# Optimization experiments

Measured on AMD Instinct MI355X. Metric: run time of the kernel, lower is better.

Reference implementation:

```python
import jax, jax.numpy as jnp
import numpy as np

B, L, D, H = 4, 2048, 512, 8
DK = D // H


def setup_inputs() -> dict:
    key = jax.random.key(0)
    ks = jax.random.split(key, 12)
    s = 1.0 / np.sqrt(D)
    return {
        "q": jax.random.normal(ks[0], (B, L, D), jnp.float32),
        "k": jax.random.normal(ks[1], (B, L, D), jnp.float32),
        "v": jax.random.normal(ks[2], (B, L, D), jnp.float32),
        "masks": jax.random.randint(ks[3], (B, L), 0, 2, jnp.int32),
        "wq_w": jax.random.normal(ks[4], (D, D), jnp.float32) * s,
        "wq_b": jnp.zeros((D,), jnp.float32),
        "wk_w": jax.random.normal(ks[5], (D, D), jnp.float32) * s,
        "wk_b": jnp.zeros((D,), jnp.float32),
        "wv_w": jax.random.normal(ks[6], (D, D), jnp.float32) * s,
        "wv_b": jnp.zeros((D,), jnp.float32),
        "wo_w": jax.random.normal(ks[7], (D, D), jnp.float32) * s,
        "wo_b": jnp.zeros((D,), jnp.float32),
    }


def reference(q, k, v, masks, wq_w, wq_b, wk_w, wk_b, wv_w, wv_b, wo_w, wo_b):
    b, l1, d = q.shape
    l2 = k.shape[1]
    # torch Linear: y = x @ W.T + b; weight shape (out, in)
    qh = (q @ wq_w.T + wq_b).reshape(b, l1, H, DK).transpose(0, 2, 1, 3)  # (B,H,L1,DK)
    kh = (k @ wk_w.T + wk_b).reshape(b, l2, H, DK).transpose(0, 2, 1, 3)  # (B,H,L2,DK)
    vh = (v @ wv_w.T + wv_b).reshape(b, l2, H, DK).transpose(0, 2, 1, 3)  # (B,H,L2,DK)
    scores = jnp.einsum("bhqd,bhkd->bhqk", qh, kh) / np.sqrt(DK).astype(np.float32)
    # 2D encoder mask (B, L2) broadcast over heads and query positions
    neg = jnp.float32(np.finfo(np.float32).min)
    scores = jnp.where(masks[:, None, None, :] == 0, neg, scores)
    weights = jax.nn.softmax(scores, axis=-1)  # dropout_rate=0.0 -> identity
    ctx = jnp.einsum("bhqk,bhkd->bhqd", weights, vh)
    concat = ctx.transpose(0, 2, 1, 3).reshape(b, l1, d)
    return concat @ wo_w.T + wo_b
```

## Files before the change

kernel.cpp:

```cpp
#include <hip/hip_runtime.h>
#include <hip/hip_bf16.h>
#include <cstddef>

typedef __attribute__((ext_vector_type(8)))  short bf16x8;
typedef __attribute__((ext_vector_type(4)))  short bf16x4;
typedef __attribute__((ext_vector_type(4)))  float f32x4;

constexpr int Bn = 4, Ln = 2048, Dn = 512, Hn = 8, DKn = 64, Mtot = 8192;
constexpr float QSCALE = 0.125f * 1.44269504088896341f;
constexpr size_t HE = (size_t)Bn * Hn * Ln * DKn;
constexpr size_t WN = (size_t)Dn * Dn;

__device__ inline unsigned cvt_pk_bf16(float lo, float hi) {
    unsigned r;
    asm("v_cvt_pk_bf16_f32 %0, %1, %2" : "=v"(r) : "v"(lo), "v"(hi));
    return r;
}
__device__ inline short f2bf(float x) {
    union { float f; unsigned u; } v; v.f = x;
    unsigned r = v.u + 0x7fffu + ((v.u >> 16) & 1u);
    return (short)(r >> 16);
}
__device__ inline void gl_lds16(const short* g, short* l) {
    __builtin_amdgcn_global_load_lds(
        (const __attribute__((address_space(1))) void*)g,
        (__attribute__((address_space(3))) void*)l, 16, 0, 0);
}

__global__ __launch_bounds__(256) void prep_all(
    const float* __restrict__ q, const float* __restrict__ k, const float* __restrict__ v,
    const float* __restrict__ wq, const float* __restrict__ wk,
    const float* __restrict__ wv, const float* __restrict__ wo,
    const int* __restrict__ masks,
    short* __restrict__ Xb, short* __restrict__ Wb, float* __restrict__ maskF)
{
    const size_t NX4 = 3 * HE / 4;
    const size_t NW4 = WN;
    size_t gid = (size_t)blockIdx.x * 256 + threadIdx.x;
    if (gid < NX4) {
        const size_t per = HE / 4;
        int which = (int)(gid >> 20);
        const float* src = (which == 0) ? q : (which == 1) ? k : v;
        size_t i4 = gid & (per - 1);
        float4 xv = *(const float4*)&src[i4 * 4];
        uint2 p = {cvt_pk_bf16(xv.x, xv.y), cvt_pk_bf16(xv.z, xv.w)};
        *(uint2*)&Xb[(size_t)which * HE + i4 * 4] = p;
    } else if (gid < NX4 + NW4) {
        size_t wi4 = gid - NX4;
        const size_t per = WN / 4;
        int which = (int)(wi4 >> 16);
        const float* src = (which == 0) ? wq : (which == 1) ? wk : (which == 2) ? wv : wo;
        size_t i4 = wi4 & (per - 1);
        float4 xv = *(const float4*)&src[i4 * 4];
        uint2 p = {cvt_pk_bf16(xv.x, xv.y), cvt_pk_bf16(xv.z, xv.w)};
        *(uint2*)&Wb[(size_t)which * WN + i4 * 4] = p;
    } else {
        size_t mi = gid - NX4 - NW4;
        if (mi < (size_t)Bn * Ln) maskF[mi] = (masks[mi] == 0) ? -1e30f : 0.f;
    }
}

__global__ __launch_bounds__(256) void mask_prep(
    const int* __restrict__ masks, float* __restrict__ maskF)
{
    int i = blockIdx.x * 256 + threadIdx.x;
    if (i < Bn * Ln) maskF[i] = (masks[i] == 0) ? -1e30f : 0.f;
}

__global__ __launch_bounds__(256) void qkv_proj_bf16(
    const short* __restrict__ Xb, const short* __restrict__ Wb,
    const float* __restrict__ bq, const float* __restrict__ bk, const float* __restrict__ bv,
    short* __restrict__ Qh, short* __restrict__ Kh, short* __restrict__ Vt)
{
    const int p = blockIdx.z;
    const short* X    = Xb + (size_t)p * Mtot * Dn;
    const short* W    = Wb + (size_t)p * Dn * Dn;
    const float* bias = (p == 0) ? bq : (p == 1) ? bk : bv;
    short*       O    = (p == 0) ? Qh : (p == 1) ? Kh : Vt;
    const float scl   = (p == 0) ? QSCALE : 1.0f;

    __shared__ short As[128 * 64];
    __shared__ short Bs[128 * 64];

    const int tid  = threadIdx.x;
    const int lane = tid & 63, w = tid >> 6;
    const int wr = w >> 1, wc = w & 1;
    const int l16 = lane & 15, g = lane >> 4;
    const int m0 = blockIdx.x * 128, n0 = blockIdx.y * 128;

    const short* Ag[4]; const short* Bg[4]; int ldsOff[4];
    #pragma unroll
    for (int f = 0; f < 4; ++f) {
        int c = tid + 256 * f;
        int row = c >> 3, col8 = c & 7;
        int scolw = ((col8 ^ (row & 7)) << 3);
        Ag[f] = X + (size_t)(m0 + row) * Dn + scolw;
        Bg[f] = W + (size_t)(n0 + row) * Dn + scolw;
        ldsOff[f] = (w * 64 + 256 * f) * 8;
    }

    f32x4 acc[4][4];
    #pragma unroll
    for (int i = 0; i < 4; ++i)
        #pragma unroll
        for (int j = 0; j < 4; ++j)
            acc[i][j] = (f32x4){0.f, 0.f, 0.f, 0.f};

    for (int ks = 0; ks < 8; ++ks) {
        #pragma unroll
        for (int f = 0; f < 4; ++f) {
            gl_lds16(Ag[f], &As[ldsOff[f]]);
            gl_lds16(Bg[f], &Bs[ldsOff[f]]);
            Ag[f] += 64; Bg[f] += 64;
        }
        __syncthreads();

        bf16x8 bfv[4][2];
        #pragma unroll
        for (int j = 0; j < 4; ++j) {
            int row = wc * 64 + j * 16 + l16;
            int sw = (row & 7) << 3;
            bfv[j][0] = *(const bf16x8*)&Bs[row * 64 + ((g * 8) ^ sw)];
            bfv[j][1] = *(const bf16x8*)&Bs[row * 64 + ((32 + g * 8) ^ sw)];
        }
        #pragma unroll
        for (int i = 0; i < 4; ++i) {
            int row = wr * 64 + i * 16 + l16;
            int sw = (row & 7) << 3;
            bf16x8 a0 = *(const bf16x8*)&As[row * 64 + ((g * 8) ^ sw)];
            bf16x8 a1 = *(const bf16x8*)&As[row * 64 + ((32 + g * 8) ^ sw)];
            #pragma unroll
            for (int j = 0; j < 4; ++j) {
                acc[i][j] = __builtin_amdgcn_mfma_f32_16x16x32_bf16(a0, bfv[j][0], acc[i][j], 0, 0, 0);
                acc[i][j] = __builtin_amdgcn_mfma_f32_16x16x32_bf16(a1, bfv[j][1], acc[i][j], 0, 0, 0);
            }
        }
        __syncthreads();
    }

    const int bb = m0 >> 11;
    #pragma unroll
    for (int i = 0; i < 4; ++i) {
        #pragma unroll
        for (int j = 0; j < 4; ++j) {
            int n  = n0 + wc * 64 + j * 16 + l16;
            int h  = n >> 6, dk = n & 63;
            float bval = bias[n];
            #pragma unroll
            for (int r = 0; r < 4; ++r) {
                int m  = m0 + wr * 64 + i * 16 + g * 4 + r;
                int lq = m & (Ln - 1);
                short val = f2bf((acc[i][j][r] + bval) * scl);
                if (p < 2)
                    O[(((size_t)bb * Hn + h) * Ln + lq) * DKn + dk] = val;
                else
                    O[(((size_t)bb * Hn + h) * DKn + dk) * Ln + lq] = val;
            }
        }
    }
}

__global__ __launch_bounds__(256) void out_proj_bf16(
    const short* __restrict__ Ctx, const short* __restrict__ Wo,
    const float* __restrict__ bias, float* __restrict__ Out)
{
    __shared__ short As[128 * 64];
    __shared__ short Bs[128 * 64];

    const int tid  = threadIdx.x;
    const int lane = tid & 63, w = tid >> 6;
    const int wr = w >> 1, wc = w & 1;
    const int l16 = lane & 15, g = lane >> 4;
    const int m0 = blockIdx.x * 128, n0 = blockIdx.y * 128;

    const short* Ag[4]; const short* Bg[4]; int ldsOff[4];
    #pragma unroll
    for (int f = 0; f < 4; ++f) {
        int c = tid + 256 * f;
        int row = c >> 3, col8 = c & 7;
        int scolw = ((col8 ^ (row & 7)) << 3);
        Ag[f] = Ctx + (size_t)(m0 + row) * Dn + scolw;
        Bg[f] = Wo  + (size_t)(n0 + row) * Dn + scolw;
        ldsOff[f] = (w * 64 + 256 * f) * 8;
    }

    f32x4 acc[4][4];
    #pragma unroll
    for (int i = 0; i < 4; ++i)
        #pragma unroll
        for (int j = 0; j < 4; ++j)
            acc[i][j] = (f32x4){0.f, 0.f, 0.f, 0.f};

    for (int ks = 0; ks < 8; ++ks) {
        #pragma unroll
        for (int f = 0; f < 4; ++f) {
            gl_lds16(Ag[f], &As[ldsOff[f]]);
            gl_lds16(Bg[f], &Bs[ldsOff[f]]);
            Ag[f] += 64; Bg[f] += 64;
        }
        __syncthreads();

        bf16x8 bfv[4][2];
        #pragma unroll
        for (int j = 0; j < 4; ++j) {
            int row = wc * 64 + j * 16 + l16;
            int sw = (row & 7) << 3;
            bfv[j][0] = *(const bf16x8*)&Bs[row * 64 + ((g * 8) ^ sw)];
            bfv[j][1] = *(const bf16x8*)&Bs[row * 64 + ((32 + g * 8) ^ sw)];
        }
        #pragma unroll
        for (int i = 0; i < 4; ++i) {
            int row = wr * 64 + i * 16 + l16;
            int sw = (row & 7) << 3;
            bf16x8 a0 = *(const bf16x8*)&As[row * 64 + ((g * 8) ^ sw)];
            bf16x8 a1 = *(const bf16x8*)&As[row * 64 + ((32 + g * 8) ^ sw)];
            #pragma unroll
            for (int j = 0; j < 4; ++j) {
                acc[i][j] = __builtin_amdgcn_mfma_f32_16x16x32_bf16(a0, bfv[j][0], acc[i][j], 0, 0, 0);
                acc[i][j] = __builtin_amdgcn_mfma_f32_16x16x32_bf16(a1, bfv[j][1], acc[i][j], 0, 0, 0);
            }
        }
        __syncthreads();
    }

    #pragma unroll
    for (int i = 0; i < 4; ++i) {
        #pragma unroll
        for (int j = 0; j < 4; ++j) {
            int n = n0 + wc * 64 + j * 16 + l16;
            float bval = bias[n];
            #pragma unroll
            for (int r = 0; r < 4; ++r) {
                int m = m0 + wr * 64 + i * 16 + g * 4 + r;
                Out[(size_t)m * Dn + n] = acc[i][j][r] + bval;
            }
        }
    }
}

__global__ __launch_bounds__(256, 4) void attn_mfma(
    const short* __restrict__ Qh, const short* __restrict__ Kh, const short* __restrict__ Vt,
    const float* __restrict__ maskF, short* __restrict__ Ctx)
{
    __shared__ short Ks[2][64 * 64];
    __shared__ short Vs[2][64 * 64];

    const int tid  = threadIdx.x;
    const int lane = tid & 63, w = tid >> 6;
    const int l16 = lane & 15, g = lane >> 4;

    const int bid = blockIdx.x;
    const int id  = (bid & 7) * 128 + (bid >> 3);
    const int qb  = id & 31;
    const int bh  = id >> 5;
    const int bb  = bh >> 3, h = bh & 7;
    const int q0  = qb * 64;
    const int NT  = Ln / 64;

    const short* Qp = Qh + (size_t)bh * Ln * DKn;
    const short* Kp = Kh + (size_t)bh * Ln * DKn;
    const short* Vp = Vt + (size_t)bh * DKn * Ln;
    const float* mp = maskF + bb * Ln;

    bf16x8 qf0 = *(const bf16x8*)&Qp[(size_t)(q0 + w * 16 + l16) * DKn + g * 8];
    bf16x8 qf1 = *(const bf16x8*)&Qp[(size_t)(q0 + w * 16 + l16) * DKn + 32 + g * 8];

    constexpr short BF1 = (short)0x3F80;
    const bf16x8 ones = {BF1, BF1, BF1, BF1, BF1, BF1, BF1, BF1};

    const int lrow = lane >> 3;
    const int scol = (((lane & 7) ^ lrow) << 3);
    const int p0r = (2 * w) * 8 + lrow, p1r = (2 * w + 1) * 8 + lrow;
    const int k0r = (p0r & 0x20) | ((p0r & 0x0C) << 1) | ((p0r & 0x10) >> 2) | (p0r & 3);
    const int k1r = (p1r & 0x20) | ((p1r & 0x0C) << 1) | ((p1r & 0x10) >> 2) | (p1r & 3);
    const short* kg0 = Kp + (size_t)k0r * DKn + scol;
    const short* kg1 = Kp + (size_t)k1r * DKn + scol;
    const short* vg0 = Vp + (size_t)p0r * Ln + scol;
    const short* vg1 = Vp + (size_t)p1r * Ln + scol;
    const int ldsb0 = (2 * w) * 512, ldsb1 = (2 * w + 1) * 512;

    int kofs[4][2];
    #pragma unroll
    for (int kt = 0; kt < 4; ++kt) {
        int row = kt * 16 + l16;
        kofs[kt][0] = row * 64 + ((g * 8) ^ ((row & 7) << 3));
        kofs[kt][1] = row * 64 + ((32 + g * 8) ^ ((row & 7) << 3));
    }

    f32x4 oacc[4];
    #pragma unroll
    for (int d = 0; d < 4; ++d) oacc[d] = (f32x4){0.f, 0.f, 0.f, 0.f};
    f32x4 lsum = (f32x4){0.f, 0.f, 0.f, 0.f};

    gl_lds16(kg0, &Ks[0][ldsb0]);
    gl_lds16(kg1, &Ks[0][ldsb1]);
    gl_lds16(vg0, &Vs[0][ldsb0]);
    gl_lds16(vg1, &Vs[0][ldsb1]);
    __syncthreads();

    int c = 0;
    for (int t = 0; t < NT; ++t) {
        if (t < NT - 1) {
            const int ko = (t + 1) * (64 * DKn);
            const int vo = (t + 1) * 64;
            gl_lds16(kg0 + ko, &Ks[c ^ 1][ldsb0]);
            gl_lds16(kg1 + ko, &Ks[c ^ 1][ldsb1]);
            gl_lds16(vg0 + vo, &Vs[c ^ 1][ldsb0]);
            gl_lds16(vg1 + vo, &Vs[c ^ 1][ldsb1]);
        }

        f32x4 mk[4];
        mk[0] = *(const f32x4*)&mp[t * 64 + 8 * g];
        mk[1] = *(const f32x4*)&mp[t * 64 + 8 * g + 4];
        mk[2] = *(const f32x4*)&mp[t * 64 + 32 + 8 * g];
        mk[3] = *(const f32x4*)&mp[t * 64 + 32 + 8 * g + 4];

        f32x4 sv[4];
        __builtin_amdgcn_s_setprio(1);
        #pragma unroll
        for (int kt = 0; kt < 4; ++kt) {
            bf16x8 kf0 = *(const bf16x8*)&Ks[c][kofs[kt][0]];
            bf16x8 kf1 = *(const bf16x8*)&Ks[c][kofs[kt][1]];
            f32x4 z = __builtin_amdgcn_mfma_f32_16x16x32_bf16(kf0, qf0, mk[kt], 0, 0, 0);
            z = __builtin_amdgcn_mfma_f32_16x16x32_bf16(kf1, qf1, z, 0, 0, 0);
            sv[kt] = z;
        }
        __builtin_amdgcn_s_setprio(0);

        bf16x8 pf[2];
        #pragma unroll
        for (int cc = 0; cc < 2; ++cc) {
            float e0 = exp2f(sv[2 * cc][0]), e1 = exp2f(sv[2 * cc][1]);
            float e2 = exp2f(sv[2 * cc][2]), e3 = exp2f(sv[2 * cc][3]);
            float e4 = exp2f(sv[2 * cc + 1][0]), e5 = exp2f(sv[2 * cc + 1][1]);
            float e6 = exp2f(sv[2 * cc + 1][2]), e7 = exp2f(sv[2 * cc + 1][3]);
            union { unsigned u[4]; bf16x8 v; } pu;
            pu.u[0] = cvt_pk_bf16(e0, e1);
            pu.u[1] = cvt_pk_bf16(e2, e3);
            pu.u[2] = cvt_pk_bf16(e4, e5);
            pu.u[3] = cvt_pk_bf16(e6, e7);
            pf[cc] = pu.v;
        }

        __builtin_amdgcn_s_setprio(1);
        #pragma unroll
        for (int cc = 0; cc < 2; ++cc) {
            lsum = __builtin_amdgcn_mfma_f32_16x16x32_bf16(ones, pf[cc], lsum, 0, 0, 0);
            #pragma unroll
            for (int d = 0; d < 4; ++d) {
                bf16x8 vf = *(const bf16x8*)&Vs[c][kofs[d][cc]];
                oacc[d] = __builtin_amdgcn_mfma_f32_16x16x32_bf16(vf, pf[cc], oacc[d], 0, 0, 0);
            }
        }
        __builtin_amdgcn_s_setprio(0);

        __syncthreads();
        c ^= 1;
    }

    float inv = 1.0f / lsum[0];
    size_t mrow = (size_t)bb * Ln + q0 + w * 16 + l16;
    #pragma unroll
    for (int d = 0; d < 4; ++d) {
        uint2 pr = {cvt_pk_bf16(oacc[d][0] * inv, oacc[d][1] * inv),
                    cvt_pk_bf16(oacc[d][2] * inv, oacc[d][3] * inv)};
        *(uint2*)&Ctx[mrow * Dn + h * 64 + d * 16 + g * 4] = pr;
    }
}

__global__ __launch_bounds__(256) void qkv_proj_mfma(
    const float* __restrict__ q, const float* __restrict__ k, const float* __restrict__ v,
    const float* __restrict__ wq, const float* __restrict__ wk, const float* __restrict__ wv,
    const float* __restrict__ bq, const float* __restrict__ bk, const float* __restrict__ bv,
    short* __restrict__ Qh, short* __restrict__ Kh, short* __restrict__ Vt)
{
    const int p = blockIdx.z;
    const float* X    = (p == 0) ? q  : (p == 1) ? k  : v;
    const float* W    = (p == 0) ? wq : (p == 1) ? wk : wv;
    const float* bias = (p == 0) ? bq : (p == 1) ? bk : bv;
    short*       O    = (p == 0) ? Qh : (p == 1) ? Kh : Vt;
    const float scl   = (p == 0) ? QSCALE : 1.0f;

    __shared__ short As[128 * 72];
    __shared__ short Bs[128 * 72];

    const int tid  = threadIdx.x;
    const int lane = tid & 63, w = tid >> 6;
    const int wr = w >> 1, wc = w & 1;
    const int l16 = lane & 15, g = lane >> 4;
    const int m0 = blockIdx.x * 128, n0 = blockIdx.y * 128;

    f32x4 acc[4][4];
    #pragma unroll
    for (int i = 0; i < 4; ++i)
        #pragma unroll
        for (int j = 0; j < 4; ++j)
            acc[i][j] = (f32x4){0.f, 0.f, 0.f, 0.f};

    for (int k0 = 0; k0 < Dn; k0 += 64) {
        #pragma unroll
        for (int f = 0; f < 8; ++f) {
            int lin = tid + 256 * f;
            int row = lin >> 4, c4 = lin & 15;
            float4 xv = *(const float4*)&X[(size_t)(m0 + row) * Dn + k0 + c4 * 4];
            uint2 xp = {cvt_pk_bf16(xv.x, xv.y), cvt_pk_bf16(xv.z, xv.w)};
            *(uint2*)&As[row * 72 + c4 * 4] = xp;
            float4 wv4 = *(const float4*)&W[(size_t)(n0 + row) * Dn + k0 + c4 * 4];
            uint2 wp = {cvt_pk_bf16(wv4.x, wv4.y), cvt_pk_bf16(wv4.z, wv4.w)};
            *(uint2*)&Bs[row * 72 + c4 * 4] = wp;
        }
        __syncthreads();

        bf16x8 af[4][2], bfv[4][2];
        #pragma unroll
        for (int i = 0; i < 4; ++i)
            #pragma unroll
            for (int c = 0; c < 2; ++c)
                af[i][c] = *(const bf16x8*)&As[(wr * 64 + i * 16 + l16) * 72 + c * 32 + g * 8];
        #pragma unroll
        for (int j = 0; j < 4; ++j)
            #pragma unroll
            for (int c = 0; c < 2; ++c)
                bfv[j][c] = *(const bf16x8*)&Bs[(wc * 64 + j * 16 + l16) * 72 + c * 32 + g * 8];

        #pragma unroll
        for (int i = 0; i < 4; ++i)
            #pragma unroll
            for (int j = 0; j < 4; ++j) {
                acc[i][j] = __builtin_amdgcn_mfma_f32_16x16x32_bf16(af[i][0], bfv[j][0], acc[i][j], 0, 0, 0);
                acc[i][j] = __builtin_amdgcn_mfma_f32_16x16x32_bf16(af[i][1], bfv[j][1], acc[i][j], 0, 0, 0);
            }
        __syncthreads();
    }

    const int bb = m0 >> 11;
    #pragma unroll
    for (int i = 0; i < 4; ++i) {
        #pragma unroll
        for (int j = 0; j < 4; ++j) {
            int n  = n0 + wc * 64 + j * 16 + l16;
            int h  = n >> 6, dk = n & 63;
            float bval = bias[n];
            #pragma unroll
            for (int r = 0; r < 4; ++r) {
                int m  = m0 + wr * 64 + i * 16 + g * 4 + r;
                int lq = m & (Ln - 1);
                short val = f2bf((acc[i][j][r] + bval) * scl);
                if (p < 2)
                    O[(((size_t)bb * Hn + h) * Ln + lq) * DKn + dk] = val;
                else
                    O[(((size_t)bb * Hn + h) * DKn + dk) * Ln + lq] = val;
            }
        }
    }
}

__global__ __launch_bounds__(256) void out_proj_mfma(
    const short* __restrict__ Ctx, const float* __restrict__ W,
    const float* __restrict__ bias, float* __restrict__ Out)
{
    __shared__ short As[128 * 72];
    __shared__ short Bs[128 * 72];

    const int tid  = threadIdx.x;
    const int lane = tid & 63, w = tid >> 6;
    const int wr = w >> 1, wc = w & 1;
    const int l16 = lane & 15, g = lane >> 4;
    const int m0 = blockIdx.x * 128, n0 = blockIdx.y * 128;

    f32x4 acc[4][4];
    #pragma unroll
    for (int i = 0; i < 4; ++i)
        #pragma unroll
        for (int j = 0; j < 4; ++j)
            acc[i][j] = (f32x4){0.f, 0.f, 0.f, 0.f};

    for (int k0 = 0; k0 < Dn; k0 += 64) {
        #pragma unroll
        for (int f = 0; f < 4; ++f) {
            int lin = tid + 256 * f;
            int row = lin >> 3, c8 = lin & 7;
            bf16x8 av = *(const bf16x8*)&Ctx[(size_t)(m0 + row) * Dn + k0 + c8 * 8];
            *(bf16x8*)&As[row * 72 + c8 * 8] = av;
        }
        #pragma unroll
        for (int f = 0; f < 8; ++f) {
            int lin = tid + 256 * f;
            int row = lin >> 4, c4 = lin & 15;
            float4 wv4 = *(const float4*)&W[(size_t)(n0 + row) * Dn + k0 + c4 * 4];
            uint2 wp = {cvt_pk_bf16(wv4.x, wv4.y), cvt_pk_bf16(wv4.z, wv4.w)};
            *(uint2*)&Bs[row * 72 + c4 * 4] = wp;
        }
        __syncthreads();

        bf16x8 af[4][2], bfv[4][2];
        #pragma unroll
        for (int i = 0; i < 4; ++i)
            #pragma unroll
            for (int c = 0; c < 2; ++c)
                af[i][c] = *(const bf16x8*)&As[(wr * 64 + i * 16 + l16) * 72 + c * 32 + g * 8];
        #pragma unroll
        for (int j = 0; j < 4; ++j)
            #pragma unroll
            for (int c = 0; c < 2; ++c)
                bfv[j][c] = *(const bf16x8*)&Bs[(wc * 64 + j * 16 + l16) * 72 + c * 32 + g * 8];

        #pragma unroll
        for (int i = 0; i < 4; ++i)
            #pragma unroll
            for (int j = 0; j < 4; ++j) {
                acc[i][j] = __builtin_amdgcn_mfma_f32_16x16x32_bf16(af[i][0], bfv[j][0], acc[i][j], 0, 0, 0);
                acc[i][j] = __builtin_amdgcn_mfma_f32_16x16x32_bf16(af[i][1], bfv[j][1], acc[i][j], 0, 0, 0);
            }
        __syncthreads();
    }

    #pragma unroll
    for (int i = 0; i < 4; ++i) {
        #pragma unroll
        for (int j = 0; j < 4; ++j) {
            int n = n0 + wc * 64 + j * 16 + l16;
            float bval = bias[n];
            #pragma unroll
            for (int r = 0; r < 4; ++r) {
                int m = m0 + wr * 64 + i * 16 + g * 4 + r;
                Out[(size_t)m * Dn + n] = acc[i][j][r] + bval;
            }
        }
    }
}

extern "C" void kernel_launch(void* const* d_in, const int* in_sizes, int n_in,
                              void* d_out, int out_size, void* d_ws, size_t ws_size,
                              hipStream_t stream)
{
    (void)in_sizes; (void)n_in; (void)out_size;
    const float* q    = (const float*)d_in[0];
    const float* k    = (const float*)d_in[1];
    const float* v    = (const float*)d_in[2];
    const int*   mks  = (const int*)  d_in[3];
    const float* wq_w = (const float*)d_in[4];
    const float* wq_b = (const float*)d_in[5];
    const float* wk_w = (const float*)d_in[6];
    const float* wk_b = (const float*)d_in[7];
    const float* wv_w = (const float*)d_in[8];
    const float* wv_b = (const float*)d_in[9];
    const float* wo_w = (const float*)d_in[10];
    const float* wo_b = (const float*)d_in[11];
    float* out = (float*)d_out;

    short* ws = (short*)d_ws;
    const size_t needed = (6 * HE + 4 * WN + 2 * (size_t)Bn * Ln) * 2;

    if (ws_size >= needed) {
        short* Xb   = ws;
        short* Ctx  = ws;
        short* Qh   = ws + 3 * HE;
        short* Kh   = ws + 4 * HE;
        short* Vt   = ws + 5 * HE;
        short* Wb   = ws + 6 * HE;
        float* maskF = (float*)(ws + 6 * HE + 4 * WN);

        const int prepBlocks = (int)((3 * HE / 4 + WN + (size_t)Bn * Ln + 255) / 256);
        prep_all<<<dim3(prepBlocks), 256, 0, stream>>>(
            q, k, v, wq_w, wk_w, wv_w, wo_w, mks, Xb, Wb, maskF);

        qkv_proj_bf16<<<dim3(64, 4, 3), 256, 0, stream>>>(
            Xb, Wb, wq_b, wk_b, wv_b, Qh, Kh, Vt);

        attn_mfma<<<dim3(1024), 256, 0, stream>>>(Qh, Kh, Vt, maskF, Ctx);

        out_proj_bf16<<<dim3(64, 4), 256, 0, stream>>>(Ctx, Wb + 3 * WN, wo_b, out);
    } else {
        short* Qh  = ws;
        short* Kh  = ws + HE;
        short* Vt  = ws + 2 * HE;
        short* Ctx = ws + 3 * HE;
        float* maskF = (float*)(ws + 4 * HE);

        mask_prep<<<dim3(32), 256, 0, stream>>>(mks, maskF);
        qkv_proj_mfma<<<dim3(Mtot / 128, Dn / 128, 3), 256, 0, stream>>>(
            q, k, v, wq_w, wk_w, wv_w, wq_b, wk_b, wv_b, Qh, Kh, Vt);
        attn_mfma<<<dim3(1024), 256, 0, stream>>>(Qh, Kh, Vt, maskF, Ctx);
        out_proj_mfma<<<dim3(Mtot / 128, Dn / 128), 256, 0, stream>>>(Ctx, wo_w, wo_b, out);
    }
}
```

Before: 120.0 us.

## Split attention KV range across wave pairs and shrink out-proj tiles

The attention kernel now has each pair of waves cover 32 queries with two M-fragments, while the two wave halves each process half of the key range (1024 keys). Partial output accumulators and row sums are merged through shared memory at the end. This improves K/V fragment reuse per LDS read but adds a reduction step and lowers launch bounds to 3 blocks per CU. The output projection moves from 128x128 to 64x64 tiles, giving 1024 blocks instead of 256 for better CU coverage, at the cost of less operand reuse per block.

```diff
diff --git a/kernel.cpp b/kernel.cpp
--- a/kernel.cpp
+++ b/kernel.cpp
@@ -3,7 +3,6 @@
 #include <cstddef>
 
 typedef __attribute__((ext_vector_type(8)))  short bf16x8;
-typedef __attribute__((ext_vector_type(4)))  short bf16x4;
 typedef __attribute__((ext_vector_type(4)))  float f32x4;
 
 constexpr int Bn = 4, Ln = 2048, Dn = 512, Hn = 8, DKn = 64, Mtot = 8192;
@@ -164,18 +163,18 @@
     const short* __restrict__ Ctx, const short* __restrict__ Wo,
     const float* __restrict__ bias, float* __restrict__ Out)
 {
-    __shared__ short As[128 * 64];
-    __shared__ short Bs[128 * 64];
+    __shared__ short As[64 * 64];
+    __shared__ short Bs[64 * 64];
 
     const int tid  = threadIdx.x;
     const int lane = tid & 63, w = tid >> 6;
     const int wr = w >> 1, wc = w & 1;
     const int l16 = lane & 15, g = lane >> 4;
-    const int m0 = blockIdx.x * 128, n0 = blockIdx.y * 128;
-
-    const short* Ag[4]; const short* Bg[4]; int ldsOff[4];
-    #pragma unroll
-    for (int f = 0; f < 4; ++f) {
+    const int m0 = blockIdx.x * 64, n0 = blockIdx.y * 64;
+
+    const short* Ag[2]; const short* Bg[2]; int ldsOff[2];
+    #pragma unroll
+    for (int f = 0; f < 2; ++f) {
         int c = tid + 256 * f;
         int row = c >> 3, col8 = c & 7;
         int scolw = ((col8 ^ (row & 7)) << 3);
@@ -184,38 +183,38 @@
         ldsOff[f] = (w * 64 + 256 * f) * 8;
     }
 
-    f32x4 acc[4][4];
-    #pragma unroll
-    for (int i = 0; i < 4; ++i)
-        #pragma unroll
-        for (int j = 0; j < 4; ++j)
+    f32x4 acc[2][2];
+    #pragma unroll
+    for (int i = 0; i < 2; ++i)
+        #pragma unroll
+        for (int j = 0; j < 2; ++j)
             acc[i][j] = (f32x4){0.f, 0.f, 0.f, 0.f};
 
     for (int ks = 0; ks < 8; ++ks) {
         #pragma unroll
-        for (int f = 0; f < 4; ++f) {
+        for (int f = 0; f < 2; ++f) {
             gl_lds16(Ag[f], &As[ldsOff[f]]);
             gl_lds16(Bg[f], &Bs[ldsOff[f]]);
             Ag[f] += 64; Bg[f] += 64;
         }
         __syncthreads();
 
-        bf16x8 bfv[4][2];
-        #pragma unroll
-        for (int j = 0; j < 4; ++j) {
-            int row = wc * 64 + j * 16 + l16;
+        bf16x8 bfv[2][2];
+        #pragma unroll
+        for (int j = 0; j < 2; ++j) {
+            int row = wc * 32 + j * 16 + l16;
             int sw = (row & 7) << 3;
             bfv[j][0] = *(const bf16x8*)&Bs[row * 64 + ((g * 8) ^ sw)];
             bfv[j][1] = *(const bf16x8*)&Bs[row * 64 + ((32 + g * 8) ^ sw)];
         }
         #pragma unroll
-        for (int i = 0; i < 4; ++i) {
-            int row = wr * 64 + i * 16 + l16;
+        for (int i = 0; i < 2; ++i) {
+            int row = wr * 32 + i * 16 + l16;
             int sw = (row & 7) << 3;
             bf16x8 a0 = *(const bf16x8*)&As[row * 64 + ((g * 8) ^ sw)];
             bf16x8 a1 = *(const bf16x8*)&As[row * 64 + ((32 + g * 8) ^ sw)];
             #pragma unroll
-            for (int j = 0; j < 4; ++j) {
+            for (int j = 0; j < 2; ++j) {
                 acc[i][j] = __builtin_amdgcn_mfma_f32_16x16x32_bf16(a0, bfv[j][0], acc[i][j], 0, 0, 0);
                 acc[i][j] = __builtin_amdgcn_mfma_f32_16x16x32_bf16(a1, bfv[j][1], acc[i][j], 0, 0, 0);
             }
@@ -224,147 +223,196 @@
     }
 
     #pragma unroll
-    for (int i = 0; i < 4; ++i) {
-        #pragma unroll
-        for (int j = 0; j < 4; ++j) {
-            int n = n0 + wc * 64 + j * 16 + l16;
+    for (int i = 0; i < 2; ++i) {
+        #pragma unroll
+        for (int j = 0; j < 2; ++j) {
+            int n = n0 + wc * 32 + j * 16 + l16;
             float bval = bias[n];
             #pragma unroll
             for (int r = 0; r < 4; ++r) {
-                int m = m0 + wr * 64 + i * 16 + g * 4 + r;
+                int m = m0 + wr * 32 + i * 16 + g * 4 + r;
                 Out[(size_t)m * Dn + n] = acc[i][j][r] + bval;
             }
         }
     }
 }
 
-__global__ __launch_bounds__(256, 4) void attn_mfma(
+__global__ __launch_bounds__(256, 3) void attn_mfma(
     const short* __restrict__ Qh, const short* __restrict__ Kh, const short* __restrict__ Vt,
     const float* __restrict__ maskF, short* __restrict__ Ctx)
 {
-    __shared__ short Ks[2][64 * 64];
-    __shared__ short Vs[2][64 * 64];
+    __shared__ short smem[16384];
 
     const int tid  = threadIdx.x;
     const int lane = tid & 63, w = tid >> 6;
     const int l16 = lane & 15, g = lane >> 4;
+    const int qt = w & 1, hf = w >> 1;
 
     const int bid = blockIdx.x;
     const int id  = (bid & 7) * 128 + (bid >> 3);
     const int qb  = id & 31;
     const int bh  = id >> 5;
-    const int bb  = bh >> 3, h = bh & 7;
+    const int bb  = bh >> 3, hd = bh & 7;
     const int q0  = qb * 64;
-    const int NT  = Ln / 64;
+    constexpr int NT = 32;
 
     const short* Qp = Qh + (size_t)bh * Ln * DKn;
     const short* Kp = Kh + (size_t)bh * Ln * DKn;
     const short* Vp = Vt + (size_t)bh * DKn * Ln;
-    const float* mp = maskF + bb * Ln;
-
-    bf16x8 qf0 = *(const bf16x8*)&Qp[(size_t)(q0 + w * 16 + l16) * DKn + g * 8];
-    bf16x8 qf1 = *(const bf16x8*)&Qp[(size_t)(q0 + w * 16 + l16) * DKn + 32 + g * 8];
+    const float* mp = maskF + bb * Ln + hf * 1024;
+
+    bf16x8 qf[2][2];
+    #pragma unroll
+    for (int mf = 0; mf < 2; ++mf)
+        #pragma unroll
+        for (int c = 0; c < 2; ++c)
+            qf[mf][c] = *(const bf16x8*)&Qp[(size_t)(q0 + qt * 32 + mf * 16 + l16) * DKn + c * 32 + g * 8];
 
     constexpr short BF1 = (short)0x3F80;
     const bf16x8 ones = {BF1, BF1, BF1, BF1, BF1, BF1, BF1, BF1};
 
-    const int lrow = lane >> 3;
-    const int scol = (((lane & 7) ^ lrow) << 3);
-    const int p0r = (2 * w) * 8 + lrow, p1r = (2 * w + 1) * 8 + lrow;
-    const int k0r = (p0r & 0x20) | ((p0r & 0x0C) << 1) | ((p0r & 0x10) >> 2) | (p0r & 3);
-    const int k1r = (p1r & 0x20) | ((p1r & 0x0C) << 1) | ((p1r & 0x10) >> 2) | (p1r & 3);
-    const short* kg0 = Kp + (size_t)k0r * DKn + scol;
-    const short* kg1 = Kp + (size_t)k1r * DKn + scol;
-    const short* vg0 = Vp + (size_t)p0r * Ln + scol;
-    const short* vg1 = Vp + (size_t)p1r * Ln + scol;
-    const int ldsb0 = (2 * w) * 512, ldsb1 = (2 * w + 1) * 512;
-
-    int kofs[4][2];
-    #pragma unroll
-    for (int kt = 0; kt < 4; ++kt) {
+    const short* kg[2]; const short* vg[2]; int sbk[2];
+    #pragma unroll
+    for (int j = 0; j < 2; ++j) {
+        int sb = qt * 2 + j;
+        sbk[j] = sb * 512;
+        int p  = sb * 8 + (lane >> 3);
+        int kc = ((p & 0x0C) << 1) | ((p & 0x10) >> 2) | (p & 3);
+        int scol = ((lane & 7) ^ (p & 7)) << 3;
+        kg[j] = Kp + (size_t)(hf * 1024 + kc) * DKn + scol;
+        int vrow = sb * 16 + (lane >> 2);
+        vg[j] = Vp + (size_t)vrow * Ln + hf * 1024 + (lane & 3) * 8;
+    }
+
+    int kofs[2][2];
+    #pragma unroll
+    for (int kt = 0; kt < 2; ++kt) {
         int row = kt * 16 + l16;
         kofs[kt][0] = row * 64 + ((g * 8) ^ ((row & 7) << 3));
         kofs[kt][1] = row * 64 + ((32 + g * 8) ^ ((row & 7) << 3));
     }
-
-    f32x4 oacc[4];
-    #pragma unroll
-    for (int d = 0; d < 4; ++d) oacc[d] = (f32x4){0.f, 0.f, 0.f, 0.f};
-    f32x4 lsum = (f32x4){0.f, 0.f, 0.f, 0.f};
-
-    gl_lds16(kg0, &Ks[0][ldsb0]);
-    gl_lds16(kg1, &Ks[0][ldsb1]);
-    gl_lds16(vg0, &Vs[0][ldsb0]);
-    gl_lds16(vg1, &Vs[0][ldsb1]);
+    int vofs[4];
+    #pragma unroll
+    for (int d = 0; d < 4; ++d)
+        vofs[d] = (d * 16 + l16) * 32 + g * 8;
+
+    f32x4 oacc[2][4];
+    #pragma unroll
+    for (int mf = 0; mf < 2; ++mf)
+        #pragma unroll
+        for (int d = 0; d < 4; ++d) oacc[mf][d] = (f32x4){0.f, 0.f, 0.f, 0.f};
+    f32x4 lsum[2] = {(f32x4){0.f, 0.f, 0.f, 0.f}, (f32x4){0.f, 0.f, 0.f, 0.f}};
+
+    #pragma unroll
+    for (int j = 0; j < 2; ++j) {
+        gl_lds16(kg[j], smem + hf * 4096 + sbk[j]);
+        gl_lds16(vg[j], smem + 8192 + hf * 4096 + sbk[j]);
+    }
     __syncthreads();
 
-    int c = 0;
+    int cb = 0;
     for (int t = 0; t < NT; ++t) {
         if (t < NT - 1) {
-            const int ko = (t + 1) * (64 * DKn);
-            const int vo = (t + 1) * 64;
-            gl_lds16(kg0 + ko, &Ks[c ^ 1][ldsb0]);
-            gl_lds16(kg1 + ko, &Ks[c ^ 1][ldsb1]);
-            gl_lds16(vg0 + vo, &Vs[c ^ 1][ldsb0]);
-            gl_lds16(vg1 + vo, &Vs[c ^ 1][ldsb1]);
-        }
-
-        f32x4 mk[4];
-        mk[0] = *(const f32x4*)&mp[t * 64 + 8 * g];
-        mk[1] = *(const f32x4*)&mp[t * 64 + 8 * g + 4];
-        mk[2] = *(const f32x4*)&mp[t * 64 + 32 + 8 * g];
-        mk[3] = *(const f32x4*)&mp[t * 64 + 32 + 8 * g + 4];
-
-        f32x4 sv[4];
+            const int ko = (t + 1) * 2048;
+            const int vo = (t + 1) * 32;
+            short* kd = smem + (hf * 2 + (cb ^ 1)) * 2048;
+            short* vd = smem + 8192 + (hf * 2 + (cb ^ 1)) * 2048;
+            #pragma unroll
+            for (int j = 0; j < 2; ++j) {
+                gl_lds16(kg[j] + ko, kd + sbk[j]);
+                gl_lds16(vg[j] + vo, vd + sbk[j]);
+            }
+        }
+        const short* Kb = smem + (hf * 2 + cb) * 2048;
+        const short* Vb = smem + 8192 + (hf * 2 + cb) * 2048;
+
+        f32x4 mk[2];
+        mk[0] = *(const f32x4*)&mp[t * 32 + 8 * g];
+        mk[1] = *(const f32x4*)&mp[t * 32 + 8 * g + 4];
+
+        bf16x8 kf[2][2];
+        #pragma unroll
+        for (int kt = 0; kt < 2; ++kt) {
+            kf[kt][0] = *(const bf16x8*)&Kb[kofs[kt][0]];
+            kf[kt][1] = *(const bf16x8*)&Kb[kofs[kt][1]];
+        }
+
+        f32x4 sv[2][2];
         __builtin_amdgcn_s_setprio(1);
         #pragma unroll
-        for (int kt = 0; kt < 4; ++kt) {
-            bf16x8 kf0 = *(const bf16x8*)&Ks[c][kofs[kt][0]];
-            bf16x8 kf1 = *(const bf16x8*)&Ks[c][kofs[kt][1]];
-            f32x4 z = __builtin_amdgcn_mfma_f32_16x16x32_bf16(kf0, qf0, mk[kt], 0, 0, 0);
-            z = __builtin_amdgcn_mfma_f32_16x16x32_bf16(kf1, qf1, z, 0, 0, 0);
-            sv[kt] = z;
-        }
+        for (int mf = 0; mf < 2; ++mf)
+            #pragma unroll
+            for (int kt = 0; kt < 2; ++kt) {
+                f32x4 z = __builtin_amdgcn_mfma_f32_16x16x32_bf16(kf[kt][0], qf[mf][0], mk[kt], 0, 0, 0);
+                z = __builtin_amdgcn_mfma_f32_16x16x32_bf16(kf[kt][1], qf[mf][1], z, 0, 0, 0);
+                sv[mf][kt] = z;
+            }
         __builtin_amdgcn_s_setprio(0);
 
         bf16x8 pf[2];
         #pragma unroll
-        for (int cc = 0; cc < 2; ++cc) {
-            float e0 = exp2f(sv[2 * cc][0]), e1 = exp2f(sv[2 * cc][1]);
-            float e2 = exp2f(sv[2 * cc][2]), e3 = exp2f(sv[2 * cc][3]);
-            float e4 = exp2f(sv[2 * cc + 1][0]), e5 = exp2f(sv[2 * cc + 1][1]);
-            float e6 = exp2f(sv[2 * cc + 1][2]), e7 = exp2f(sv[2 * cc + 1][3]);
+        for (int mf = 0; mf < 2; ++mf) {
+            float e0 = exp2f(sv[mf][0][0]), e1 = exp2f(sv[mf][0][1]);
+            float e2 = exp2f(sv[mf][0][2]), e3 = exp2f(sv[mf][0][3]);
+            float e4 = exp2f(sv[mf][1][0]), e5 = exp2f(sv[mf][1][1]);
+            float e6 = exp2f(sv[mf][1][2]), e7 = exp2f(sv[mf][1][3]);
             union { unsigned u[4]; bf16x8 v; } pu;
             pu.u[0] = cvt_pk_bf16(e0, e1);
             pu.u[1] = cvt_pk_bf16(e2, e3);
             pu.u[2] = cvt_pk_bf16(e4, e5);
             pu.u[3] = cvt_pk_bf16(e6, e7);
-            pf[cc] = pu.v;
-        }
+            pf[mf] = pu.v;
+        }
+
+        bf16x8 vf[4];
+        #pragma unroll
+        for (int d = 0; d < 4; ++d)
+            vf[d] = *(const bf16x8*)&Vb[vofs[d]];
 
         __builtin_amdgcn_s_setprio(1);
         #pragma unroll
-        for (int cc = 0; cc < 2; ++cc) {
-            lsum = __builtin_amdgcn_mfma_f32_16x16x32_bf16(ones, pf[cc], lsum, 0, 0, 0);
+        for (int mf = 0; mf < 2; ++mf) {
+            lsum[mf] = __builtin_amdgcn_mfma_f32_16x16x32_bf16(ones, pf[mf], lsum[mf], 0, 0, 0);
+            #pragma unroll
+            for (int d = 0; d < 4; ++d)
+                oacc[mf][d] = __builtin_amdgcn_mfma_f32_16x16x32_bf16(vf[d], pf[mf], oacc[mf][d], 0, 0, 0);
+        }
+        __builtin_amdgcn_s_setprio(0);
+
+        __syncthreads();
+        cb ^= 1;
+    }
+
+    float* M = (float*)smem;
+    if (hf == 1) {
+        #pragma unroll
+        for (int mf = 0; mf < 2; ++mf) {
+            int ql = qt * 32 + mf * 16 + l16;
+            #pragma unroll
+            for (int d = 0; d < 4; ++d)
+                *(f32x4*)&M[ql * 68 + d * 16 + g * 4] = oacc[mf][d];
+            if (g == 0) M[ql * 68 + 64] = lsum[mf][0];
+        }
+    }
+    __syncthreads();
+    if (hf == 0) {
+        #pragma unroll
+        for (int mf = 0; mf < 2; ++mf) {
+            int ql = qt * 32 + mf * 16 + l16;
+            float lt = lsum[mf][0] + M[ql * 68 + 64];
+            float inv = 1.0f / lt;
+            size_t mrow = (size_t)bb * Ln + q0 + ql;
             #pragma unroll
             for (int d = 0; d < 4; ++d) {
-                bf16x8 vf = *(const bf16x8*)&Vs[c][kofs[d][cc]];
-                oacc[d] = __builtin_amdgcn_mfma_f32_16x16x32_bf16(vf, pf[cc], oacc[d], 0, 0, 0);
-            }
-        }
-        __builtin_amdgcn_s_setprio(0);
-
-        __syncthreads();
-        c ^= 1;
-    }
-
-    float inv = 1.0f / lsum[0];
-    size_t mrow = (size_t)bb * Ln + q0 + w * 16 + l16;
-    #pragma unroll
-    for (int d = 0; d < 4; ++d) {
-        uint2 pr = {cvt_pk_bf16(oacc[d][0] * inv, oacc[d][1] * inv),
-                    cvt_pk_bf16(oacc[d][2] * inv, oacc[d][3] * inv)};
-        *(uint2*)&Ctx[mrow * Dn + h * 64 + d * 16 + g * 4] = pr;
+                f32x4 ob = *(const f32x4*)&M[ql * 68 + d * 16 + g * 4];
+                float o0 = (oacc[mf][d][0] + ob[0]) * inv;
+                float o1 = (oacc[mf][d][1] + ob[1]) * inv;
+                float o2 = (oacc[mf][d][2] + ob[2]) * inv;
+                float o3 = (oacc[mf][d][3] + ob[3]) * inv;
+                uint2 pr = {cvt_pk_bf16(o0, o1), cvt_pk_bf16(o2, o3)};
+                *(uint2*)&Ctx[mrow * Dn + hd * 64 + d * 16 + g * 4] = pr;
+            }
+        }
     }
 }
 
@@ -570,7 +618,7 @@
 
         attn_mfma<<<dim3(1024), 256, 0, stream>>>(Qh, Kh, Vt, maskF, Ctx);
 
-        out_proj_bf16<<<dim3(64, 4), 256, 0, stream>>>(Ctx, Wb + 3 * WN, wo_b, out);
+        out_proj_bf16<<<dim3(128, 8), 256, 0, stream>>>(Ctx, Wb + 3 * WN, wo_b, out);
     } else {
         short* Qh  = ws;
         short* Kh  = ws + HE;
```

Result: faster. 114.9 us (-4.3%).
